# Performance work log

Measured on AMD Instinct MI355X. Metric: run time of the kernel, lower is better.

Reference implementation:

```python
import jax, jax.numpy as jnp
import numpy as np

NUM_EXPERTS = 8
TOP_K = 2
D = 2048   # hidden_dim
F = 4096   # ffn_dim


def setup_inputs() -> dict:
    key = jax.random.key(0)
    k0, k1, k2, k3, k4 = jax.random.split(key, 5)
    hidden_states = jax.random.normal(k0, (2, 2048, D), dtype=jnp.float32)
    gate_w = jax.random.normal(k1, (NUM_EXPERTS, D), dtype=jnp.float32) * 0.02
    w1 = jax.random.normal(k2, (NUM_EXPERTS, F, D), dtype=jnp.float32) * 0.02
    w2 = jax.random.normal(k3, (NUM_EXPERTS, D, F), dtype=jnp.float32) * 0.02
    w3 = jax.random.normal(k4, (NUM_EXPERTS, F, D), dtype=jnp.float32) * 0.02
    return {"hidden_states": hidden_states, "gate_w": gate_w, "w1": w1, "w2": w2, "w3": w3}


def reference(hidden_states, gate_w, w1, w2, w3):
    B, S, Dm = hidden_states.shape
    h = hidden_states.reshape(-1, Dm)                      # [T, D]
    router_logits = h @ gate_w.T                           # [T, E]
    rw = jax.nn.softmax(router_logits.astype(jnp.float32), axis=-1)
    rw, selected = jax.lax.top_k(rw, TOP_K)                # [T, K], [T, K]
    rw = rw / jnp.sum(rw, axis=-1, keepdims=True)
    rw = rw.astype(h.dtype)
    final = jnp.zeros_like(h)
    for e in range(NUM_EXPERTS):                            # small fixed loop over experts
        w = jnp.sum(rw * (selected == e), axis=1, keepdims=True)  # [T, 1]
        gated = jax.nn.silu(h @ w1[e].T) * (h @ w3[e].T)   # [T, F]
        final = final + (gated @ w2[e].T) * w              # [T, D]
    return final.reshape(B, S, Dm), router_logits
```

## Files before the change

### kernel.cpp

```cpp
#include <hip/hip_runtime.h>
#include <hip/hip_bf16.h>
#include <stdint.h>

#define NE 8
#define TKK 2
#define DD 2048
#define FF 4096
#define TT 4096
#define NCB 49152

typedef __attribute__((ext_vector_type(8))) short bf16x8;
typedef __attribute__((ext_vector_type(4))) float f32x4;

__device__ inline unsigned short f2bf(float f) {
  union { float f; unsigned u; } x; x.f = f;
  unsigned r = x.u + 0x7fffu + ((x.u >> 16) & 1u);
  return (unsigned short)(r >> 16);
}

__device__ inline bf16x8 cvt8(float4 a, float4 b) {
  union { unsigned short h[8]; bf16x8 v; } x;
  x.h[0] = f2bf(a.x); x.h[1] = f2bf(a.y); x.h[2] = f2bf(a.z); x.h[3] = f2bf(a.w);
  x.h[4] = f2bf(b.x); x.h[5] = f2bf(b.y); x.h[6] = f2bf(b.z); x.h[7] = f2bf(b.w);
  return x.v;
}

__device__ __forceinline__ void conv16(const float* __restrict__ src,
                                       unsigned short* __restrict__ dst, long i) {
  float4 a0 = *(const float4*)(src + i);
  float4 a1 = *(const float4*)(src + i + 4);
  float4 a2 = *(const float4*)(src + i + 8);
  float4 a3 = *(const float4*)(src + i + 12);
  union { unsigned short h[8]; uint4 v; } o0, o1;
  o0.h[0] = f2bf(a0.x); o0.h[1] = f2bf(a0.y); o0.h[2] = f2bf(a0.z); o0.h[3] = f2bf(a0.w);
  o0.h[4] = f2bf(a1.x); o0.h[5] = f2bf(a1.y); o0.h[6] = f2bf(a1.z); o0.h[7] = f2bf(a1.w);
  o1.h[0] = f2bf(a2.x); o1.h[1] = f2bf(a2.y); o1.h[2] = f2bf(a2.z); o1.h[3] = f2bf(a2.w);
  o1.h[4] = f2bf(a3.x); o1.h[5] = f2bf(a3.y); o1.h[6] = f2bf(a3.z); o1.h[7] = f2bf(a3.w);
  *(uint4*)(dst + i) = o0.v;
  *(uint4*)(dst + i + 8) = o1.v;
}

__device__ inline void conv8(const float* __restrict__ src,
                             unsigned short* __restrict__ dst, long i) {
  float4 a = *(const float4*)(src + i);
  float4 b = *(const float4*)(src + i + 4);
  union { unsigned short h[8]; uint4 v; } o;
  o.h[0] = f2bf(a.x); o.h[1] = f2bf(a.y); o.h[2] = f2bf(a.z); o.h[3] = f2bf(a.w);
  o.h[4] = f2bf(b.x); o.h[5] = f2bf(b.y); o.h[6] = f2bf(b.z); o.h[7] = f2bf(b.w);
  *(uint4*)(dst + i) = o.v;
}

#define GLL16(g, l) __builtin_amdgcn_global_load_lds( \
    (__attribute__((address_space(1))) void*)(void*)(g), \
    (__attribute__((address_space(3))) void*)(l), 16, 0, 0)

#define LDV(p) (*(const bf16x8*)(p))
#define MF(d, a, b) d = __builtin_amdgcn_mfma_f32_16x16x32_bf16(a, b, d, 0, 0, 0)
#define BARPH() do { asm volatile("" ::: "memory"); __builtin_amdgcn_s_barrier(); \
                     __builtin_amdgcn_sched_barrier(0); } while (0)

__device__ __forceinline__ void router_one(
    int t, int lane, const float* __restrict__ h, const float* __restrict__ gw,
    float* __restrict__ logits, unsigned short* __restrict__ hb,
    int* __restrict__ counts, int* __restrict__ tok_idx,
    int* __restrict__ sel_e, int* __restrict__ sel_slot, float* __restrict__ sel_w) {
  const float4* hr = (const float4*)(h + (size_t)t * DD);
  float4 hv[8];
  float acc[NE];
#pragma unroll
  for (int e = 0; e < NE; e++) acc[e] = 0.f;
#pragma unroll
  for (int j = 0; j < 8; j++) hv[j] = hr[j * 64 + lane];
  ushort4* hbr = (ushort4*)(hb + (size_t)t * DD);
#pragma unroll
  for (int j = 0; j < 8; j++) {
    ushort4 o;
    o.x = f2bf(hv[j].x); o.y = f2bf(hv[j].y); o.z = f2bf(hv[j].z); o.w = f2bf(hv[j].w);
    hbr[j * 64 + lane] = o;
  }
#pragma unroll
  for (int e = 0; e < NE; e++) {
    const float4* g = (const float4*)(gw + (size_t)e * DD);
    float a = 0.f;
#pragma unroll
    for (int j = 0; j < 8; j++) {
      float4 gv = g[j * 64 + lane];
      a += hv[j].x * gv.x + hv[j].y * gv.y + hv[j].z * gv.z + hv[j].w * gv.w;
    }
    acc[e] = a;
  }
#pragma unroll
  for (int e = 0; e < NE; e++) {
    float v = acc[e];
#pragma unroll
    for (int o = 32; o > 0; o >>= 1) v += __shfl_xor(v, o, 64);
    acc[e] = v;
  }
  if (lane == 0) {
#pragma unroll
    for (int e = 0; e < NE; e++) logits[(size_t)t * NE + e] = acc[e];
    int e1 = 0; float m1 = acc[0];
#pragma unroll
    for (int e = 1; e < NE; e++) if (acc[e] > m1) { m1 = acc[e]; e1 = e; }
    int e2 = -1; float m2 = -3.4e38f;
#pragma unroll
    for (int e = 0; e < NE; e++) if (e != e1 && acc[e] > m2) { m2 = acc[e]; e2 = e; }
    float s = expf(m2 - m1);
    float wa = 1.f / (1.f + s);
    float wb = s * wa;
    int s1 = atomicAdd(&counts[e1], 1);
    tok_idx[e1 * TT + s1] = t;
    int s2 = atomicAdd(&counts[e2], 1);
    tok_idx[e2 * TT + s2] = t;
    sel_e[2 * t] = e1; sel_slot[2 * t] = s1; sel_w[2 * t] = wa;
    sel_e[2 * t + 1] = e2; sel_slot[2 * t + 1] = s2; sel_w[2 * t + 1] = wb;
  }
}

__global__ void router_kernel(const float* __restrict__ h, const float* __restrict__ gw,
                              float* __restrict__ logits, unsigned short* __restrict__ hb,
                              int* __restrict__ counts, int* __restrict__ tok_idx,
                              int* __restrict__ sel_e, int* __restrict__ sel_slot,
                              float* __restrict__ sel_w) {
  router_one(blockIdx.x, threadIdx.x, h, gw, logits, hb, counts, tok_idx, sel_e, sel_slot, sel_w);
}

__global__ __launch_bounds__(256) void prep_kernel(
    const float* __restrict__ h, const float* __restrict__ gw,
    float* __restrict__ logits, unsigned short* __restrict__ hb,
    int* __restrict__ counts, int* __restrict__ tok_idx,
    int* __restrict__ sel_e, int* __restrict__ sel_slot, float* __restrict__ sel_w,
    const float* __restrict__ w1, unsigned short* __restrict__ w1b,
    const float* __restrict__ w3, unsigned short* __restrict__ w3b,
    const float* __restrict__ w2, unsigned short* __restrict__ w2b) {
  int b = blockIdx.x;
  if (b < NCB) {
    int t = b >> 14;
    long j = ((long)(b & 16383) * 256 + threadIdx.x) * 16;
    const float* src = (t == 0) ? w1 : (t == 1) ? w3 : w2;
    unsigned short* dst = (t == 0) ? w1b : (t == 1) ? w3b : w2b;
    conv16(src, dst, j);
    return;
  }
  int rb = b - NCB;
  router_one(rb * 4 + (threadIdx.x >> 6), threadIdx.x & 63,
             h, gw, logits, hb, counts, tok_idx, sel_e, sel_slot, sel_w);
}

__global__ void offsets_kernel(const int* __restrict__ counts, int* __restrict__ offsets) {
  if (threadIdx.x == 0) {
    int r = 0;
    for (int e = 0; e < NE; e++) { offsets[e] = r; r += counts[e]; }
  }
}


__global__ __launch_bounds__(512, 2) void gemm1_8p(
    const unsigned short* __restrict__ w1b, const unsigned short* __restrict__ w3b,
    const unsigned short* __restrict__ hb, const int* __restrict__ tok_idx,
    const int* __restrict__ counts, const int* __restrict__ offsets,
    unsigned short* __restrict__ gated) {
  __shared__ __align__(16) char lds[131072];

  int bid = blockIdx.x;
  int x = bid & 7, rest = bid >> 3;
  int m = rest & 15, q = rest >> 4;
  int p = x + 8 * q;
  int n = p & 31, e = p >> 5;
  int cnt = counts[e];
  int row0 = m * 256;
  if (row0 >= cnt) return;
  int offe = offsets[e];
  int tid = threadIdx.x;
  int lane = tid & 63;
  int wv = tid >> 6;
  int wm = wv >> 2, wn = wv & 3;

  int swz = ((tid & 7) ^ ((tid >> 3) & 7)) * 8;
  long asrc[4];
#pragma unroll
  for (int i = 0; i < 4; i++) {
    int r = i * 64 + (tid >> 3);
    int rr = row0 + r; if (rr >= cnt) rr = cnt - 1;
    int tok = tok_idx[e * TT + rr];
    asrc[i] = (long)tok * DD + swz;
  }
  int fbase = n * 128;
  long ebw = (long)e * FF * DD;
  long bs[2];
#pragma unroll
  for (int i = 0; i < 2; i++) {
    int r = i * 64 + (tid >> 3);
    bs[i] = ebw + (long)(fbase + r) * DD + swz;
  }

#define G1A(c, i, ko)  GLL16(hb  + asrc[i] + (ko), lds +           (c) * 32768 + (i) * 8192 + tid * 16)
#define G1B1(c, i, ko) GLL16(w1b + bs[i]   + (ko), lds + 65536 +  (c) * 16384 + (i) * 8192 + tid * 16)
#define G1B3(c, i, ko) GLL16(w3b + bs[i]   + (ko), lds + 98304 +  (c) * 16384 + (i) * 8192 + tid * 16)

  int arow[8], brow[2];
#pragma unroll
  for (int i = 0; i < 8; i++) arow[i] = (wm * 128 + i * 16 + (lane & 15)) * 128;
#pragma unroll
  for (int j = 0; j < 2; j++) brow[j] = (wn * 32 + j * 16 + (lane & 15)) * 128;
  int kx0 = (((lane >> 4)) ^ (lane & 7)) * 16;
  int kx1 = ((4 + (lane >> 4)) ^ (lane & 7)) * 16;

  f32x4 acc1[8][2], acc3[8][2];
#pragma unroll
  for (int i = 0; i < 8; i++)
#pragma unroll
    for (int j = 0; j < 2; j++) { acc1[i][j] = (f32x4){0,0,0,0}; acc3[i][j] = (f32x4){0,0,0,0}; }

  G1A(0, 0, 0); G1A(0, 2, 0);
  G1B1(0, 0, 0); G1B1(0, 1, 0);
  G1B3(0, 0, 0); G1B3(0, 1, 0);
  G1A(0, 1, 0); G1A(0, 3, 0);

  int cur = 0;
  bf16x8 b10, b11, b30, b31;
  for (int kt = 0; kt < DD / 64; kt++) {
    int ko = (kt + 1) * 64;
    bool st = (kt < DD / 64 - 1);
    int nc = cur ^ 1;
    const char* Ac  = lds + cur * 32768;
    const char* B1c = lds + 65536 + cur * 16384;
    const char* B3c = lds + 98304 + cur * 16384;

    asm volatile("s_waitcnt vmcnt(2)" ::: "memory");
    BARPH();
    if (st) { G1A(nc, 0, ko); G1A(nc, 2, ko); }
    b10 = LDV(B1c + brow[0] + kx0); b11 = LDV(B1c + brow[1] + kx0);
    b30 = LDV(B3c + brow[0] + kx0); b31 = LDV(B3c + brow[1] + kx0);
    __builtin_amdgcn_s_setprio(1);
#pragma unroll
    for (int i = 0; i < 4; i++) {
      bf16x8 av = LDV(Ac + arow[i] + kx0);
      MF(acc1[i][0], av, b10); MF(acc1[i][1], av, b11);
      MF(acc3[i][0], av, b30); MF(acc3[i][1], av, b31);
    }
    __builtin_amdgcn_s_setprio(0);

    if (st) asm volatile("s_waitcnt vmcnt(2)" ::: "memory");
    else    asm volatile("s_waitcnt vmcnt(0)" ::: "memory");
    BARPH();
    if (st) { G1B1(nc, 0, ko); G1B1(nc, 1, ko); }
    __builtin_amdgcn_s_setprio(1);
#pragma unroll
    for (int i = 4; i < 8; i++) {
      bf16x8 av = LDV(Ac + arow[i] + kx0);
      MF(acc1[i][0], av, b10); MF(acc1[i][1], av, b11);
      MF(acc3[i][0], av, b30); MF(acc3[i][1], av, b31);
    }
    __builtin_amdgcn_s_setprio(0);

    BARPH();
    if (st) { G1B3(nc, 0, ko); G1B3(nc, 1, ko); }
    b10 = LDV(B1c + brow[0] + kx1); b11 = LDV(B1c + brow[1] + kx1);
    b30 = LDV(B3c + brow[0] + kx1); b31 = LDV(B3c + brow[1] + kx1);
    __builtin_amdgcn_s_setprio(1);
#pragma unroll
    for (int i = 0; i < 4; i++) {
      bf16x8 av = LDV(Ac + arow[i] + kx1);
      MF(acc1[i][0], av, b10); MF(acc1[i][1], av, b11);
      MF(acc3[i][0], av, b30); MF(acc3[i][1], av, b31);
    }
    __builtin_amdgcn_s_setprio(0);

    BARPH();
    if (st) { G1A(nc, 1, ko); G1A(nc, 3, ko); }
    __builtin_amdgcn_s_setprio(1);
#pragma unroll
    for (int i = 4; i < 8; i++) {
      bf16x8 av = LDV(Ac + arow[i] + kx1);
      MF(acc1[i][0], av, b10); MF(acc1[i][1], av, b11);
      MF(acc3[i][0], av, b30); MF(acc3[i][1], av, b31);
    }
    __builtin_amdgcn_s_setprio(0);
    cur = nc;
  }

  int r0 = wm * 128 + ((lane >> 4) << 2);
  int c0 = fbase + wn * 32 + (lane & 15);
#pragma unroll
  for (int i = 0; i < 8; i++)
#pragma unroll
    for (int j = 0; j < 2; j++)
#pragma unroll
      for (int r = 0; r < 4; r++) {
        int tr = r0 + i * 16 + r;
        if (row0 + tr < cnt) {
          float g = acc1[i][j][r];
          float sg = g / (1.f + __expf(-g));
          gated[(size_t)(offe + row0 + tr) * FF + (c0 + j * 16)] = f2bf(sg * acc3[i][j][r]);
        }
      }
}

__global__ __launch_bounds__(512, 2) void gemm2_8p(
    const unsigned short* __restrict__ w2b, const unsigned short* __restrict__ gated,
    const int* __restrict__ counts, const int* __restrict__ offsets,
    float* __restrict__ eout) {
  __shared__ __align__(16) char lds[98304];

  int bid = blockIdx.x;
  int x = bid & 7, rest = bid >> 3;
  int m = rest & 15, q = rest >> 4;
  int p = x + 8 * q;
  int n = p & 15, e = p >> 4;
  int cnt = counts[e];
  int row0 = m * 256;
  if (row0 >= cnt) return;
  int offe = offsets[e];
  int tid = threadIdx.x;
  int lane = tid & 63;
  int wv = tid >> 6;
  int wm = wv >> 2, wn = wv & 3;

  int swz = ((tid & 7) ^ ((tid >> 3) & 7)) * 8;
  long asrc[4];
#pragma unroll
  for (int i = 0; i < 4; i++) {
    int r = i * 64 + (tid >> 3);
    int rr = row0 + r; if (rr >= cnt) rr = cnt - 1;
    asrc[i] = (long)(offe + rr) * FF + swz;
  }
  int dbase = n * 128;
  long ebw = (long)e * DD * FF;
  long bs[2];
#pragma unroll
  for (int i = 0; i < 2; i++) {
    int r = i * 64 + (tid >> 3);
    bs[i] = ebw + (long)(dbase + r) * FF + swz;
  }

#define G2A(c, i, ko) GLL16(gated + asrc[i] + (ko), lds +          (c) * 32768 + (i) * 8192 + tid * 16)
#define G2B(c, i, ko) GLL16(w2b   + bs[i]   + (ko), lds + 65536 + (c) * 16384 + (i) * 8192 + tid * 16)

  int arow[8], brow[2];
#pragma unroll
  for (int i = 0; i < 8; i++) arow[i] = (wm * 128 + i * 16 + (lane & 15)) * 128;
#pragma unroll
  for (int j = 0; j < 2; j++) brow[j] = (wn * 32 + j * 16 + (lane & 15)) * 128;
  int kx0 = (((lane >> 4)) ^ (lane & 7)) * 16;
  int kx1 = ((4 + (lane >> 4)) ^ (lane & 7)) * 16;

  f32x4 acc[8][2];
#pragma unroll
  for (int i = 0; i < 8; i++)
#pragma unroll
    for (int j = 0; j < 2; j++) acc[i][j] = (f32x4){0,0,0,0};

  G2A(0, 0, 0); G2A(0, 2, 0);
  G2B(0, 0, 0); G2B(0, 1, 0);
  G2A(0, 1, 0); G2A(0, 3, 0);

  int cur = 0;
  bf16x8 b0, b1;
  for (int kt = 0; kt < FF / 64; kt++) {
    int ko = (kt + 1) * 64;
    bool st = (kt < FF / 64 - 1);
    int nc = cur ^ 1;
    const char* Ac = lds + cur * 32768;
    const char* Bc = lds + 65536 + cur * 16384;

    asm volatile("s_waitcnt vmcnt(2)" ::: "memory");
    BARPH();
    if (st) { G2A(nc, 0, ko); G2A(nc, 2, ko); }
    b0 = LDV(Bc + brow[0] + kx0); b1 = LDV(Bc + brow[1] + kx0);
    __builtin_amdgcn_s_setprio(1);
#pragma unroll
    for (int i = 0; i < 4; i++) {
      bf16x8 av = LDV(Ac + arow[i] + kx0);
      MF(acc[i][0], av, b0); MF(acc[i][1], av, b1);
    }
    __builtin_amdgcn_s_setprio(0);

    if (st) asm volatile("s_waitcnt vmcnt(2)" ::: "memory");
    else    asm volatile("s_waitcnt vmcnt(0)" ::: "memory");
    BARPH();
    if (st) { G2B(nc, 0, ko); G2B(nc, 1, ko); }
    __builtin_amdgcn_s_setprio(1);
#pragma unroll
    for (int i = 4; i < 8; i++) {
      bf16x8 av = LDV(Ac + arow[i] + kx0);
      MF(acc[i][0], av, b0); MF(acc[i][1], av, b1);
    }
    __builtin_amdgcn_s_setprio(0);

    BARPH();
    if (st) { G2A(nc, 1, ko); G2A(nc, 3, ko); }
    b0 = LDV(Bc + brow[0] + kx1); b1 = LDV(Bc + brow[1] + kx1);
    __builtin_amdgcn_s_setprio(1);
#pragma unroll
    for (int i = 0; i < 4; i++) {
      bf16x8 av = LDV(Ac + arow[i] + kx1);
      MF(acc[i][0], av, b0); MF(acc[i][1], av, b1);
    }
    __builtin_amdgcn_s_setprio(0);

    BARPH();
    __builtin_amdgcn_s_setprio(1);
#pragma unroll
    for (int i = 4; i < 8; i++) {
      bf16x8 av = LDV(Ac + arow[i] + kx1);
      MF(acc[i][0], av, b0); MF(acc[i][1], av, b1);
    }
    __builtin_amdgcn_s_setprio(0);
    cur = nc;
  }

  int r0 = wm * 128 + ((lane >> 4) << 2);
  int c0 = dbase + wn * 32 + (lane & 15);
#pragma unroll
  for (int i = 0; i < 8; i++)
#pragma unroll
    for (int j = 0; j < 2; j++)
#pragma unroll
      for (int r = 0; r < 4; r++) {
        int tr = r0 + i * 16 + r;
        if (row0 + tr < cnt)
          eout[(size_t)(offe + row0 + tr) * DD + (c0 + j * 16)] = acc[i][j][r];
      }
}

__global__ __launch_bounds__(256) void gemm1_kernel_fb(
    const float* __restrict__ w1f, const float* __restrict__ w3f,
    const unsigned short* __restrict__ hb, const int* __restrict__ tok_idx,
    const int* __restrict__ counts, const int* __restrict__ offsets,
    unsigned short* __restrict__ gated) {
  __shared__ __align__(16) char lds[49152];
  char* Ab = lds;
  char* B1 = lds + 16384;
  char* B3 = lds + 32768;

  int bid = blockIdx.x;
  int x = bid & 7;
  int rest = bid >> 3;
  int m = rest & 31;
  int q = rest >> 5;
  int p = x + 8 * q;
  int n = p & 63;
  int e = p >> 6;
  int cnt = counts[e];
  int row0 = m * 128;
  if (row0 >= cnt) return;
  int offe = offsets[e];
  int tid = threadIdx.x;

  long asrc[4];
#pragma unroll
  for (int i = 0; i < 4; i++) {
    int r = i * 32 + (tid >> 3);
    int rr = row0 + r; if (rr >= cnt) rr = cnt - 1;
    int tok = tok_idx[e * TT + rr];
    asrc[i] = (long)tok * DD + (((tid & 7) ^ (r & 7)) * 8);
  }
  int fbase = n * 64;
  long ebase = (long)e * FF * DD;
  long bsrc[4];
#pragma unroll
  for (int i = 0; i < 4; i++) {
    int r = i * 16 + (tid >> 4);
    bsrc[i] = ebase + (long)(fbase + r) * DD + (((tid & 15) ^ (r & 15)) * 4);
  }

  f32x4 acc1[4][2], acc3[4][2];
#pragma unroll
  for (int i = 0; i < 4; i++)
#pragma unroll
    for (int j = 0; j < 2; j++) { acc1[i][j] = (f32x4){0,0,0,0}; acc3[i][j] = (f32x4){0,0,0,0}; }

  int wv = tid >> 6;
  int lane = tid & 63;
  int wr = (wv >> 1) * 64;
  int wc = (wv & 1) * 32;
  int lrow = lane & 15;
  int lk4 = lane >> 4;

  for (int k0 = 0; k0 < DD; k0 += 64) {
    if (k0) __syncthreads();
#pragma unroll
    for (int i = 0; i < 4; i++)
      GLL16(hb + asrc[i] + k0, Ab + i * 4096 + tid * 16);
#pragma unroll
    for (int i = 0; i < 4; i++) {
      GLL16(w1f + bsrc[i] + k0, B1 + i * 4096 + tid * 16);
      GLL16(w3f + bsrc[i] + k0, B3 + i * 4096 + tid * 16);
    }
    __syncthreads();
#pragma unroll
    for (int kk = 0; kk < 2; kk++) {
      int kseg = kk * 4 + lk4;
      int fs = kk * 8 + lk4 * 2;
      bf16x8 af[4], b1f[2], b3f[2];
#pragma unroll
      for (int i = 0; i < 4; i++) {
        int row = wr + i * 16 + lrow;
        af[i] = *(const bf16x8*)(Ab + row * 128 + ((kseg ^ (row & 7)) * 16));
      }
#pragma unroll
      for (int j = 0; j < 2; j++) {
        int row = wc + j * 16 + lrow;
        int rx = row & 15;
        float4 a0 = *(const float4*)(B1 + row * 256 + ((fs ^ rx) * 16));
        float4 a1 = *(const float4*)(B1 + row * 256 + (((fs + 1) ^ rx) * 16));
        b1f[j] = cvt8(a0, a1);
        float4 c0 = *(const float4*)(B3 + row * 256 + ((fs ^ rx) * 16));
        float4 c1 = *(const float4*)(B3 + row * 256 + (((fs + 1) ^ rx) * 16));
        b3f[j] = cvt8(c0, c1);
      }
#pragma unroll
      for (int i = 0; i < 4; i++)
#pragma unroll
        for (int j = 0; j < 2; j++) {
          acc1[i][j] = __builtin_amdgcn_mfma_f32_16x16x32_bf16(af[i], b1f[j], acc1[i][j], 0, 0, 0);
          acc3[i][j] = __builtin_amdgcn_mfma_f32_16x16x32_bf16(af[i], b3f[j], acc3[i][j], 0, 0, 0);
        }
    }
  }
  int crow0 = wr + (lane >> 4) * 4;
  int ccol0 = wc + (lane & 15);
#pragma unroll
  for (int i = 0; i < 4; i++)
#pragma unroll
    for (int j = 0; j < 2; j++)
#pragma unroll
      for (int r = 0; r < 4; r++) {
        int trow = crow0 + i * 16 + r;
        if (row0 + trow < cnt) {
          float g = acc1[i][j][r];
          float sg = g / (1.f + __expf(-g));
          float val = sg * acc3[i][j][r];
          gated[(size_t)(offe + row0 + trow) * FF + (fbase + ccol0 + j * 16)] = f2bf(val);
        }
      }
}

__global__ __launch_bounds__(256) void gemm2_kernel_fb(
    const float* __restrict__ w2f, const unsigned short* __restrict__ gated,
    const int* __restrict__ counts, const int* __restrict__ offsets,
    float* __restrict__ eout) {
  __shared__ __align__(16) char lds[49152];
  char* Ab = lds;
  char* Bb = lds + 16384;

  int bid = blockIdx.x;
  int x = bid & 7;
  int rest = bid >> 3;
  int m = rest & 31;
  int q = rest >> 5;
  int p = x + 8 * q;
  int n = p & 15;
  int e = p >> 4;
  int cnt = counts[e];
  int row0 = m * 128;
  if (row0 >= cnt) return;
  int offe = offsets[e];
  int tid = threadIdx.x;

  long asrc[4];
#pragma unroll
  for (int i = 0; i < 4; i++) {
    int r = i * 32 + (tid >> 3);
    int rr = row0 + r; if (rr >= cnt) rr = cnt - 1;
    asrc[i] = (long)(offe + rr) * FF + (((tid & 7) ^ (r & 7)) * 8);
  }
  int dbase = n * 128;
  long ebase = (long)e * DD * FF;
  long bsrc[8];
#pragma unroll
  for (int i = 0; i < 8; i++) {
    int r = i * 16 + (tid >> 4);
    bsrc[i] = ebase + (long)(dbase + r) * FF + (((tid & 15) ^ (r & 15)) * 4);
  }

  f32x4 acc[4][4];
#pragma unroll
  for (int i = 0; i < 4; i++)
#pragma unroll
    for (int j = 0; j < 4; j++) acc[i][j] = (f32x4){0,0,0,0};

  int wv = tid >> 6;
  int lane = tid & 63;
  int wr = (wv >> 1) * 64;
  int wc = (wv & 1) * 64;
  int lrow = lane & 15;
  int lk4 = lane >> 4;

  for (int k0 = 0; k0 < FF; k0 += 64) {
    if (k0) __syncthreads();
#pragma unroll
    for (int i = 0; i < 4; i++)
      GLL16(gated + asrc[i] + k0, Ab + i * 4096 + tid * 16);
#pragma unroll
    for (int i = 0; i < 8; i++)
      GLL16(w2f + bsrc[i] + k0, Bb + i * 4096 + tid * 16);
    __syncthreads();
#pragma unroll
    for (int kk = 0; kk < 2; kk++) {
      int kseg = kk * 4 + lk4;
      int fs = kk * 8 + lk4 * 2;
      bf16x8 af[4], bf[4];
#pragma unroll
      for (int i = 0; i < 4; i++) {
        int row = wr + i * 16 + lrow;
        af[i] = *(const bf16x8*)(Ab + row * 128 + ((kseg ^ (row & 7)) * 16));
      }
#pragma unroll
      for (int j = 0; j < 4; j++) {
        int row = wc + j * 16 + lrow;
        int rx = row & 15;
        float4 a0 = *(const float4*)(Bb + row * 256 + ((fs ^ rx) * 16));
        float4 a1 = *(const float4*)(Bb + row * 256 + (((fs + 1) ^ rx) * 16));
        bf[j] = cvt8(a0, a1);
      }
#pragma unroll
      for (int i = 0; i < 4; i++)
#pragma unroll
        for (int j = 0; j < 4; j++)
          acc[i][j] = __builtin_amdgcn_mfma_f32_16x16x32_bf16(af[i], bf[j], acc[i][j], 0, 0, 0);
    }
  }
  int crow0 = wr + (lane >> 4) * 4;
  int ccol0 = wc + (lane & 15);
#pragma unroll
  for (int i = 0; i < 4; i++)
#pragma unroll
    for (int j = 0; j < 4; j++)
#pragma unroll
      for (int r = 0; r < 4; r++) {
        int trow = crow0 + i * 16 + r;
        if (row0 + trow < cnt)
          eout[(size_t)(offe + row0 + trow) * DD + (dbase + ccol0 + j * 16)] = acc[i][j][r];
      }
}

__global__ void gather_kernel(const float* __restrict__ eout, const int* __restrict__ offsets,
                              const int* __restrict__ sel_e, const int* __restrict__ sel_slot,
                              const float* __restrict__ sel_w, float* __restrict__ out) {
  int idx = blockIdx.x * 256 + threadIdx.x;
  int t = idx >> 9;
  int c = idx & 511;
  int ea = sel_e[2 * t], eb = sel_e[2 * t + 1];
  int sa = offsets[ea] + sel_slot[2 * t];
  int sb = offsets[eb] + sel_slot[2 * t + 1];
  float wa = sel_w[2 * t], wb = sel_w[2 * t + 1];
  float4 va = ((const float4*)(eout + (size_t)sa * DD))[c];
  float4 vb = ((const float4*)(eout + (size_t)sb * DD))[c];
  float4 o;
  o.x = wa * va.x + wb * vb.x;
  o.y = wa * va.y + wb * vb.y;
  o.z = wa * va.z + wb * vb.z;
  o.w = wa * va.w + wb * vb.w;
  ((float4*)(out + (size_t)t * DD))[c] = o;
}

extern "C" void kernel_launch(void* const* d_in, const int* in_sizes, int n_in,
                              void* d_out, int out_size, void* d_ws, size_t ws_size,
                              hipStream_t stream) {
  const float* h  = (const float*)d_in[0];
  const float* gw = (const float*)d_in[1];
  const float* w1 = (const float*)d_in[2];
  const float* w2 = (const float*)d_in[3];
  const float* w3 = (const float*)d_in[4];
  float* out = (float*)d_out;
  float* logits = out + (size_t)TT * DD;

  char* wp = (char*)d_ws;
  int* counts = (int*)wp; wp += 256;
  int* offsets = (int*)wp; wp += 256;
  int* tok_idx = (int*)wp; wp += (size_t)NE * TT * 4;
  int* sel_e = (int*)wp; wp += (size_t)TT * 2 * 4;
  int* sel_slot = (int*)wp; wp += (size_t)TT * 2 * 4;
  float* sel_w = (float*)wp; wp += (size_t)TT * 2 * 4;
  unsigned short* hb = (unsigned short*)wp; wp += (size_t)TT * DD * 2;
  unsigned short* gated = (unsigned short*)wp; wp += (size_t)TT * TKK * FF * 2;
  float* eout = (float*)wp; wp += (size_t)TT * TKK * DD * 4;
  if ((size_t)(wp - (char*)d_ws) > ws_size) return;

  long nw = (long)NE * FF * DD;
  unsigned short* w1b = (unsigned short*)wp; wp += (size_t)nw * 2;
  unsigned short* w3b = (unsigned short*)wp; wp += (size_t)nw * 2;
  unsigned short* w2b = (unsigned short*)wp; wp += (size_t)nw * 2;
  bool wb16 = ((size_t)(wp - (char*)d_ws) <= ws_size);

  hipMemsetAsync(counts, 0, 32, stream);
  if (wb16) {
    prep_kernel<<<NCB + TT / 4, 256, 0, stream>>>(
        h, gw, logits, hb, counts, tok_idx, sel_e, sel_slot, sel_w,
        w1, w1b, w3, w3b, w2, w2b);
    offsets_kernel<<<1, 64, 0, stream>>>(counts, offsets);
    gemm1_8p<<<8 * 16 * 32, 512, 0, stream>>>(w1b, w3b, hb, tok_idx, counts, offsets, gated);
    gemm2_8p<<<8 * 16 * 16, 512, 0, stream>>>(w2b, gated, counts, offsets, eout);
  } else {
    router_kernel<<<TT, 64, 0, stream>>>(h, gw, logits, hb, counts, tok_idx, sel_e, sel_slot, sel_w);
    offsets_kernel<<<1, 64, 0, stream>>>(counts, offsets);
    gemm1_kernel_fb<<<8 * 32 * 64, 256, 0, stream>>>(w1, w3, hb, tok_idx, counts, offsets, gated);
    gemm2_kernel_fb<<<8 * 32 * 16, 256, 0, stream>>>(w2, gated, counts, offsets, eout);
  }
  gather_kernel<<<(TT * DD / 4) / 256, 256, 0, stream>>>(eout, offsets, sel_e, sel_slot, sel_w, out);
}
```

Baseline: 861.4 us.

## Batch LDS fragment loads ahead of MFMAs and store expert outputs as bf16

Restructures the gemm1 and gemm2 main loops so each phase issues all LDS fragment reads up front, waits on lgkmcnt once, then runs its MFMAs. Global-to-LDS prefetch issue is reordered and gemm2 drops from four barrier phases per k-step to two. Expert outputs are now written as bf16 instead of fp32, which halves eout traffic, and the gather kernel reads 8 bf16 values per thread. This adds register pressure from the held fragments and a bf16 rounding step before the final weighted combine.

```diff
diff --git a/kernel.cpp b/kernel.cpp
--- a/kernel.cpp
+++ b/kernel.cpp
@@ -16,6 +16,10 @@
   union { float f; unsigned u; } x; x.f = f;
   unsigned r = x.u + 0x7fffu + ((x.u >> 16) & 1u);
   return (unsigned short)(r >> 16);
+}
+
+__device__ inline float bf2f(unsigned short v) {
+  union { unsigned u; float f; } x; x.u = (unsigned)v << 16; return x.f;
 }
 
 __device__ inline bf16x8 cvt8(float4 a, float4 b) {
@@ -40,24 +44,17 @@
   *(uint4*)(dst + i + 8) = o1.v;
 }
 
-__device__ inline void conv8(const float* __restrict__ src,
-                             unsigned short* __restrict__ dst, long i) {
-  float4 a = *(const float4*)(src + i);
-  float4 b = *(const float4*)(src + i + 4);
-  union { unsigned short h[8]; uint4 v; } o;
-  o.h[0] = f2bf(a.x); o.h[1] = f2bf(a.y); o.h[2] = f2bf(a.z); o.h[3] = f2bf(a.w);
-  o.h[4] = f2bf(b.x); o.h[5] = f2bf(b.y); o.h[6] = f2bf(b.z); o.h[7] = f2bf(b.w);
-  *(uint4*)(dst + i) = o.v;
-}
-
 #define GLL16(g, l) __builtin_amdgcn_global_load_lds( \
     (__attribute__((address_space(1))) void*)(void*)(g), \
     (__attribute__((address_space(3))) void*)(l), 16, 0, 0)
 
 #define LDV(p) (*(const bf16x8*)(p))
 #define MF(d, a, b) d = __builtin_amdgcn_mfma_f32_16x16x32_bf16(a, b, d, 0, 0, 0)
-#define BARPH() do { asm volatile("" ::: "memory"); __builtin_amdgcn_s_barrier(); \
-                     __builtin_amdgcn_sched_barrier(0); } while (0)
+#define WAITVN(n) asm volatile("s_waitcnt vmcnt(" #n ")" ::: "memory")
+#define WAITL0() do { asm volatile("s_waitcnt lgkmcnt(0)" ::: "memory"); \
+                      __builtin_amdgcn_sched_barrier(0); } while (0)
+#define BAR() do { asm volatile("" ::: "memory"); __builtin_amdgcn_s_barrier(); \
+                   asm volatile("" ::: "memory"); } while (0)
 
 __device__ __forceinline__ void router_one(
     int t, int lane, const float* __restrict__ h, const float* __restrict__ gw,
@@ -218,7 +215,6 @@
   G1A(0, 1, 0); G1A(0, 3, 0);
 
   int cur = 0;
-  bf16x8 b10, b11, b30, b31;
   for (int kt = 0; kt < DD / 64; kt++) {
     int ko = (kt + 1) * 64;
     bool st = (kt < DD / 64 - 1);
@@ -226,55 +222,63 @@
     const char* Ac  = lds + cur * 32768;
     const char* B1c = lds + 65536 + cur * 16384;
     const char* B3c = lds + 98304 + cur * 16384;
-
-    asm volatile("s_waitcnt vmcnt(2)" ::: "memory");
-    BARPH();
+    bf16x8 a[4];
+
+    WAITVN(2);
+    BAR();
+    bf16x8 b10k0 = LDV(B1c + brow[0] + kx0), b11k0 = LDV(B1c + brow[1] + kx0);
+    bf16x8 b30k0 = LDV(B3c + brow[0] + kx0), b31k0 = LDV(B3c + brow[1] + kx0);
+#pragma unroll
+    for (int i = 0; i < 4; i++) a[i] = LDV(Ac + arow[i] + kx0);
     if (st) { G1A(nc, 0, ko); G1A(nc, 2, ko); }
-    b10 = LDV(B1c + brow[0] + kx0); b11 = LDV(B1c + brow[1] + kx0);
-    b30 = LDV(B3c + brow[0] + kx0); b31 = LDV(B3c + brow[1] + kx0);
+    WAITL0();
     __builtin_amdgcn_s_setprio(1);
 #pragma unroll
     for (int i = 0; i < 4; i++) {
-      bf16x8 av = LDV(Ac + arow[i] + kx0);
-      MF(acc1[i][0], av, b10); MF(acc1[i][1], av, b11);
-      MF(acc3[i][0], av, b30); MF(acc3[i][1], av, b31);
+      MF(acc1[i][0], a[i], b10k0); MF(acc1[i][1], a[i], b11k0);
+      MF(acc3[i][0], a[i], b30k0); MF(acc3[i][1], a[i], b31k0);
     }
     __builtin_amdgcn_s_setprio(0);
-
-    if (st) asm volatile("s_waitcnt vmcnt(2)" ::: "memory");
-    else    asm volatile("s_waitcnt vmcnt(0)" ::: "memory");
-    BARPH();
+    BAR();
+
+    bf16x8 b10k1 = LDV(B1c + brow[0] + kx1), b11k1 = LDV(B1c + brow[1] + kx1);
+    bf16x8 b30k1 = LDV(B3c + brow[0] + kx1), b31k1 = LDV(B3c + brow[1] + kx1);
+#pragma unroll
+    for (int i = 0; i < 4; i++) a[i] = LDV(Ac + arow[i] + kx1);
     if (st) { G1B1(nc, 0, ko); G1B1(nc, 1, ko); }
+    WAITL0();
     __builtin_amdgcn_s_setprio(1);
 #pragma unroll
-    for (int i = 4; i < 8; i++) {
-      bf16x8 av = LDV(Ac + arow[i] + kx0);
-      MF(acc1[i][0], av, b10); MF(acc1[i][1], av, b11);
-      MF(acc3[i][0], av, b30); MF(acc3[i][1], av, b31);
+    for (int i = 0; i < 4; i++) {
+      MF(acc1[i][0], a[i], b10k1); MF(acc1[i][1], a[i], b11k1);
+      MF(acc3[i][0], a[i], b30k1); MF(acc3[i][1], a[i], b31k1);
     }
     __builtin_amdgcn_s_setprio(0);
 
-    BARPH();
+    if (st) WAITVN(4); else WAITVN(0);
+    BAR();
+#pragma unroll
+    for (int i = 0; i < 4; i++) a[i] = LDV(Ac + arow[4 + i] + kx0);
     if (st) { G1B3(nc, 0, ko); G1B3(nc, 1, ko); }
-    b10 = LDV(B1c + brow[0] + kx1); b11 = LDV(B1c + brow[1] + kx1);
-    b30 = LDV(B3c + brow[0] + kx1); b31 = LDV(B3c + brow[1] + kx1);
+    WAITL0();
     __builtin_amdgcn_s_setprio(1);
 #pragma unroll
     for (int i = 0; i < 4; i++) {
-      bf16x8 av = LDV(Ac + arow[i] + kx1);
-      MF(acc1[i][0], av, b10); MF(acc1[i][1], av, b11);
-      MF(acc3[i][0], av, b30); MF(acc3[i][1], av, b31);
+      MF(acc1[4 + i][0], a[i], b10k0); MF(acc1[4 + i][1], a[i], b11k0);
+      MF(acc3[4 + i][0], a[i], b30k0); MF(acc3[4 + i][1], a[i], b31k0);
     }
     __builtin_amdgcn_s_setprio(0);
-
-    BARPH();
+    BAR();
+
+#pragma unroll
+    for (int i = 0; i < 4; i++) a[i] = LDV(Ac + arow[4 + i] + kx1);
     if (st) { G1A(nc, 1, ko); G1A(nc, 3, ko); }
+    WAITL0();
     __builtin_amdgcn_s_setprio(1);
 #pragma unroll
-    for (int i = 4; i < 8; i++) {
-      bf16x8 av = LDV(Ac + arow[i] + kx1);
-      MF(acc1[i][0], av, b10); MF(acc1[i][1], av, b11);
-      MF(acc3[i][0], av, b30); MF(acc3[i][1], av, b31);
+    for (int i = 0; i < 4; i++) {
+      MF(acc1[4 + i][0], a[i], b10k1); MF(acc1[4 + i][1], a[i], b11k1);
+      MF(acc3[4 + i][0], a[i], b30k1); MF(acc3[4 + i][1], a[i], b31k1);
     }
     __builtin_amdgcn_s_setprio(0);
     cur = nc;
@@ -300,7 +304,7 @@
 __global__ __launch_bounds__(512, 2) void gemm2_8p(
     const unsigned short* __restrict__ w2b, const unsigned short* __restrict__ gated,
     const int* __restrict__ counts, const int* __restrict__ offsets,
-    float* __restrict__ eout) {
+    unsigned short* __restrict__ eout) {
   __shared__ __align__(16) char lds[98304];
 
   int bid = blockIdx.x;
@@ -356,55 +360,41 @@
   G2A(0, 1, 0); G2A(0, 3, 0);
 
   int cur = 0;
-  bf16x8 b0, b1;
   for (int kt = 0; kt < FF / 64; kt++) {
     int ko = (kt + 1) * 64;
     bool st = (kt < FF / 64 - 1);
     int nc = cur ^ 1;
     const char* Ac = lds + cur * 32768;
     const char* Bc = lds + 65536 + cur * 16384;
-
-    asm volatile("s_waitcnt vmcnt(2)" ::: "memory");
-    BARPH();
-    if (st) { G2A(nc, 0, ko); G2A(nc, 2, ko); }
-    b0 = LDV(Bc + brow[0] + kx0); b1 = LDV(Bc + brow[1] + kx0);
+    bf16x8 a0[4], a1v[4];
+
+    WAITVN(2);
+    BAR();
+    bf16x8 b0 = LDV(Bc + brow[0] + kx0), b1 = LDV(Bc + brow[1] + kx0);
+    bf16x8 b2 = LDV(Bc + brow[0] + kx1), b3 = LDV(Bc + brow[1] + kx1);
+#pragma unroll
+    for (int i = 0; i < 4; i++) { a0[i] = LDV(Ac + arow[i] + kx0); a1v[i] = LDV(Ac + arow[i] + kx1); }
+    if (st) { G2A(nc, 0, ko); G2A(nc, 2, ko); G2B(nc, 0, ko); G2B(nc, 1, ko); }
+    WAITL0();
     __builtin_amdgcn_s_setprio(1);
 #pragma unroll
     for (int i = 0; i < 4; i++) {
-      bf16x8 av = LDV(Ac + arow[i] + kx0);
-      MF(acc[i][0], av, b0); MF(acc[i][1], av, b1);
+      MF(acc[i][0], a0[i], b0); MF(acc[i][1], a0[i], b1);
+      MF(acc[i][0], a1v[i], b2); MF(acc[i][1], a1v[i], b3);
     }
     __builtin_amdgcn_s_setprio(0);
 
-    if (st) asm volatile("s_waitcnt vmcnt(2)" ::: "memory");
-    else    asm volatile("s_waitcnt vmcnt(0)" ::: "memory");
-    BARPH();
-    if (st) { G2B(nc, 0, ko); G2B(nc, 1, ko); }
+    if (st) WAITVN(4); else WAITVN(0);
+    BAR();
+#pragma unroll
+    for (int i = 0; i < 4; i++) { a0[i] = LDV(Ac + arow[4 + i] + kx0); a1v[i] = LDV(Ac + arow[4 + i] + kx1); }
+    if (st) { G2A(nc, 1, ko); G2A(nc, 3, ko); }
+    WAITL0();
     __builtin_amdgcn_s_setprio(1);
 #pragma unroll
-    for (int i = 4; i < 8; i++) {
-      bf16x8 av = LDV(Ac + arow[i] + kx0);
-      MF(acc[i][0], av, b0); MF(acc[i][1], av, b1);
-    }
-    __builtin_amdgcn_s_setprio(0);
-
-    BARPH();
-    if (st) { G2A(nc, 1, ko); G2A(nc, 3, ko); }
-    b0 = LDV(Bc + brow[0] + kx1); b1 = LDV(Bc + brow[1] + kx1);
-    __builtin_amdgcn_s_setprio(1);
-#pragma unroll
     for (int i = 0; i < 4; i++) {
-      bf16x8 av = LDV(Ac + arow[i] + kx1);
-      MF(acc[i][0], av, b0); MF(acc[i][1], av, b1);
-    }
-    __builtin_amdgcn_s_setprio(0);
-
-    BARPH();
-    __builtin_amdgcn_s_setprio(1);
-#pragma unroll
-    for (int i = 4; i < 8; i++) {
-      bf16x8 av = LDV(Ac + arow[i] + kx1);
-      MF(acc[i][0], av, b0); MF(acc[i][1], av, b1);
+      MF(acc[4 + i][0], a0[i], b0); MF(acc[4 + i][1], a0[i], b1);
+      MF(acc[4 + i][0], a1v[i], b2); MF(acc[4 + i][1], a1v[i], b3);
     }
     __builtin_amdgcn_s_setprio(0);
     cur = nc;
@@ -420,7 +410,7 @@
       for (int r = 0; r < 4; r++) {
         int tr = r0 + i * 16 + r;
         if (row0 + tr < cnt)
-          eout[(size_t)(offe + row0 + tr) * DD + (c0 + j * 16)] = acc[i][j][r];
+          eout[(size_t)(offe + row0 + tr) * DD + (c0 + j * 16)] = f2bf(acc[i][j][r]);
       }
 }
 
@@ -540,7 +530,7 @@
 __global__ __launch_bounds__(256) void gemm2_kernel_fb(
     const float* __restrict__ w2f, const unsigned short* __restrict__ gated,
     const int* __restrict__ counts, const int* __restrict__ offsets,
-    float* __restrict__ eout) {
+    unsigned short* __restrict__ eout) {
   __shared__ __align__(16) char lds[49152];
   char* Ab = lds;
   char* Bb = lds + 16384;
@@ -632,28 +622,35 @@
       for (int r = 0; r < 4; r++) {
         int trow = crow0 + i * 16 + r;
         if (row0 + trow < cnt)
-          eout[(size_t)(offe + row0 + trow) * DD + (dbase + ccol0 + j * 16)] = acc[i][j][r];
+          eout[(size_t)(offe + row0 + trow) * DD + (dbase + ccol0 + j * 16)] = f2bf(acc[i][j][r]);
       }
 }
 
-__global__ void gather_kernel(const float* __restrict__ eout, const int* __restrict__ offsets,
+__global__ void gather_kernel(const unsigned short* __restrict__ eout, const int* __restrict__ offsets,
                               const int* __restrict__ sel_e, const int* __restrict__ sel_slot,
                               const float* __restrict__ sel_w, float* __restrict__ out) {
   int idx = blockIdx.x * 256 + threadIdx.x;
-  int t = idx >> 9;
-  int c = idx & 511;
+  int t = idx >> 8;
+  int c = (idx & 255) * 8;
   int ea = sel_e[2 * t], eb = sel_e[2 * t + 1];
-  int sa = offsets[ea] + sel_slot[2 * t];
-  int sb = offsets[eb] + sel_slot[2 * t + 1];
+  long sa = (long)(offsets[ea] + sel_slot[2 * t]) * DD + c;
+  long sb = (long)(offsets[eb] + sel_slot[2 * t + 1]) * DD + c;
   float wa = sel_w[2 * t], wb = sel_w[2 * t + 1];
-  float4 va = ((const float4*)(eout + (size_t)sa * DD))[c];
-  float4 vb = ((const float4*)(eout + (size_t)sb * DD))[c];
-  float4 o;
-  o.x = wa * va.x + wb * vb.x;
-  o.y = wa * va.y + wb * vb.y;
-  o.z = wa * va.z + wb * vb.z;
-  o.w = wa * va.w + wb * vb.w;
-  ((float4*)(out + (size_t)t * DD))[c] = o;
+  union { uint4 v; unsigned short h[8]; } va, vb;
+  va.v = *(const uint4*)(eout + sa);
+  vb.v = *(const uint4*)(eout + sb);
+  float4 o0, o1;
+  o0.x = wa * bf2f(va.h[0]) + wb * bf2f(vb.h[0]);
+  o0.y = wa * bf2f(va.h[1]) + wb * bf2f(vb.h[1]);
+  o0.z = wa * bf2f(va.h[2]) + wb * bf2f(vb.h[2]);
+  o0.w = wa * bf2f(va.h[3]) + wb * bf2f(vb.h[3]);
+  o1.x = wa * bf2f(va.h[4]) + wb * bf2f(vb.h[4]);
+  o1.y = wa * bf2f(va.h[5]) + wb * bf2f(vb.h[5]);
+  o1.z = wa * bf2f(va.h[6]) + wb * bf2f(vb.h[6]);
+  o1.w = wa * bf2f(va.h[7]) + wb * bf2f(vb.h[7]);
+  float* op = out + (size_t)t * DD + c;
+  *(float4*)op = o0;
+  *(float4*)(op + 4) = o1;
 }
 
 extern "C" void kernel_launch(void* const* d_in, const int* in_sizes, int n_in,
@@ -676,7 +673,7 @@
   float* sel_w = (float*)wp; wp += (size_t)TT * 2 * 4;
   unsigned short* hb = (unsigned short*)wp; wp += (size_t)TT * DD * 2;
   unsigned short* gated = (unsigned short*)wp; wp += (size_t)TT * TKK * FF * 2;
-  float* eout = (float*)wp; wp += (size_t)TT * TKK * DD * 4;
+  unsigned short* eout = (unsigned short*)wp; wp += (size_t)TT * TKK * DD * 2;
   if ((size_t)(wp - (char*)d_ws) > ws_size) return;
 
   long nw = (long)NE * FF * DD;
@@ -699,5 +696,5 @@
     gemm1_kernel_fb<<<8 * 32 * 64, 256, 0, stream>>>(w1, w3, hb, tok_idx, counts, offsets, gated);
     gemm2_kernel_fb<<<8 * 32 * 16, 256, 0, stream>>>(w2, gated, counts, offsets, eout);
   }
-  gather_kernel<<<(TT * DD / 4) / 256, 256, 0, stream>>>(eout, offsets, sel_e, sel_slot, sel_w, out);
-}
+  gather_kernel<<<TT * DD / 8 / 256, 256, 0, stream>>>(eout, offsets, sel_e, sel_slot, sel_w, out);
+}
```

Result: no change. 846.2 us (-1.8%).
